# Performance work log

Measured on AMD Instinct MI355X. Metric: run time of the kernel, lower is better.

## Reference

```python
import jax, jax.numpy as jnp
import numpy as np

B, C, H, W = 1, 448, 64, 64
K, M, PAD, STRIDE = 7, 7, 3, 1
CG = C // K          # key/query channels (KeyQueryMap divides by k) = 64
GP_HID = int(0.5 * CG)  # geometry prior hidden channels = 32
K2 = K * K
CENTER = K2 // 2


def conv1x1(x, w, b):
    # x: (B, Cin, H, W), w: (Cout, Cin), b: (Cout,)
    return jnp.einsum('bchw,oc->bohw', x, w) + b[None, :, None, None]


def unfold(x):
    # torch.nn.Unfold(K, dilation=1, padding=PAD, stride=STRIDE)
    # output layout: (B, Cin*K2, L) with dim1 index = c*K2 + (di*K + dj)
    Bc, Cc, Hc, Wc = x.shape
    xp = jnp.pad(x, ((0, 0), (0, 0), (PAD, PAD), (PAD, PAD)))
    Ho = (Hc + 2 * PAD - K) // STRIDE + 1
    Wo = (Wc + 2 * PAD - K) // STRIDE + 1
    patches = [xp[:, :, di:di + Ho * STRIDE:STRIDE, dj:dj + Wo * STRIDE:STRIDE]
               for di in range(K) for dj in range(K)]
    u = jnp.stack(patches, axis=2)  # (B, Cc, K2, Ho, Wo)
    return u.reshape(Bc, Cc * K2, Ho * Wo), Ho, Wo


def geometry_prior(gp_w1, gp_b1, gp_w2, gp_b2):
    ar = jnp.arange(-(K // 2), K // 2 + 1, dtype=jnp.float32)   # -3..3
    x_pos = jnp.broadcast_to(ar[None, :], (K, K))
    y_pos = jnp.broadcast_to(ar[::-1][:, None], (K, K))          # 3..-3 down rows
    pos = jnp.stack([x_pos, y_pos], axis=0)[None]                # (1, 2, K, K)
    h = jax.nn.relu(conv1x1(pos, gp_w1, gp_b1))
    out = conv1x1(h, gp_w2, gp_b2)                               # (1, CG, K, K)
    return out.reshape(1, CG, 1, K2)


def setup_inputs() -> dict:
    key = jax.random.key(0)
    ks = jax.random.split(key, 12)
    def lin(k, cout, cin):
        return jax.random.normal(k, (cout, cin), jnp.float32) / np.sqrt(cin)
    inp = {
        'x': jax.random.normal(ks[0], (B, C, H, W), jnp.float32),
        'Wk': lin(ks[1], CG, C), 'bk': jnp.zeros((CG,), jnp.float32),
        'Wq': lin(ks[2], CG, C), 'bq': jnp.zeros((CG,), jnp.float32),
        'gp_w1': lin(ks[3], GP_HID, 2), 'gp_b1': jax.random.normal(ks[4], (GP_HID,), jnp.float32) * 0.01,
        'gp_w2': lin(ks[5], CG, GP_HID), 'gp_b2': jax.random.normal(ks[6], (CG,), jnp.float32) * 0.01,
        'Wf': lin(ks[7], C, C), 'bf': jnp.zeros((C,), jnp.float32),
    }
    return inp


def reference(x, Wk, bk, Wq, bq, gp_w1, gp_b1, gp_w2, gp_b2, Wf, bf):
    gpk = geometry_prior(gp_w1, gp_b1, gp_w2, gp_b2)        # (1, CG, 1, K2)
    km = conv1x1(x, Wk, bk)                                  # (B, CG, H, W)
    qm = conv1x1(x, Wq, bq)
    ku, Ho, Wo = unfold(km)
    L = Ho * Wo
    ku = ku.reshape(B, CG, L, K2)   # same row-major semantics as torch .view
    qu, _, _ = unfold(qm)
    qu = qu.reshape(B, CG, L, K2)
    ak = ku * qu[:, :, :, CENTER:CENTER + 1]                 # (B, CG, L, K2)
    ck = jax.nn.softmax(ak + gpk, axis=-1)                   # (B, CG, L, K2)
    xu, _, _ = unfold(x)
    xu = xu.reshape(B, M, C // M, L, K2)                     # (B, M, CG, L, K2)
    # ck broadcasts over the M axis (valid since B == 1); sum over window dim
    pre = jnp.einsum('bglp,bmglp->bmgl', ck, xu).reshape(B, C, Ho, Wo)
    return conv1x1(pre, Wf, bf)
```

## Files before the change

### kernel.cpp

```cpp
#include <hip/hip_runtime.h>
#include <hip/hip_bf16.h>

#define CC   448
#define CGC  64
#define MMM  7
#define HWSZ 4096
#define KK2  49
#define GPH  32

typedef __attribute__((ext_vector_type(8))) short   short8;
typedef __attribute__((ext_vector_type(4))) float   f32x4;
typedef __attribute__((ext_vector_type(4))) unsigned short us4;

__device__ __forceinline__ unsigned short f2b(float f) {
    union { __hip_bfloat16 h; unsigned short u; } cv;
    cv.h = __float2bfloat16(f);
    return cv.u;
}

__global__ __launch_bounds__(1024, 4) void kq_mfma(
    const float* __restrict__ x,
    const float* __restrict__ Wk, const float* __restrict__ bk,
    const float* __restrict__ Wq, const float* __restrict__ bq,
    float* __restrict__ km, float* __restrict__ qm)
{
    __shared__ unsigned short As[57344];
    __shared__ unsigned short Bs[7168];
    __shared__ float         red[2048];

    const int tid  = threadIdx.x;
    const int nT   = blockIdx.x * 16;
    const int lane = tid & 63;
    const int wid  = tid >> 6;
    const int l15  = lane & 15;
    const int l4   = lane >> 4;

    #pragma unroll
    for (int i = 0; i < 14; ++i) {
        int idx = tid + i * 1024;
        int row = idx / 112;
        int c   = idx - row * 112;
        const float* src = (row < 64) ? (Wk + (size_t)row * CC)
                                      : (Wq + (size_t)(row - 64) * CC);
        float4 v = *(const float4*)(src + c * 4);
        int kg = c >> 1, jo = (c & 1) * 4;
        *(us4*)&As[kg * 1024 + row * 8 + jo] =
            (us4){ f2b(v.x), f2b(v.y), f2b(v.z), f2b(v.w) };
    }
    #pragma unroll
    for (int i = 0; i < 2; ++i) {
        int idx = tid + i * 1024;
        if (idx < 1792) {
            int row = idx >> 2, c4 = idx & 3;
            float4 v = *(const float4*)(x + (size_t)row * HWSZ + nT + c4 * 4);
            int kg = row >> 3, j = row & 7;
            int b  = kg * 128 + c4 * 32 + j;
            Bs[b]      = f2b(v.x);
            Bs[b + 8]  = f2b(v.y);
            Bs[b + 16] = f2b(v.z);
            Bs[b + 24] = f2b(v.w);
        }
    }
    __syncthreads();

    const int mt = (wid & 7) * 16;
    const int kh = wid >> 3;
    f32x4 acc = (f32x4){0.f, 0.f, 0.f, 0.f};
    #pragma unroll
    for (int i = 0; i < 7; ++i) {
        int K4 = kh * 28 + i * 4;
        short8 fa = *(short8*)&As[(K4 + l4) * 1024 + (mt + l15) * 8];
        short8 fb = *(short8*)&Bs[(K4 + l4) * 128 + l15 * 8];
        acc = __builtin_amdgcn_mfma_f32_16x16x32_bf16(fa, fb, acc, 0, 0, 0);
    }
    if (kh == 1)
        *(f32x4*)&red[(wid & 7) * 256 + lane * 4] = acc;
    __syncthreads();
    if (kh == 0) {
        f32x4 o = *(f32x4*)&red[(wid & 7) * 256 + lane * 4];
        const bool isK = (mt < 64);
        float*       Cd   = isK ? km : qm;
        const float* bias = isK ? bk : bq;
        const int rb = (mt & 63) + l4 * 4;
        #pragma unroll
        for (int r = 0; r < 4; ++r) {
            int row = rb + r;
            Cd[(size_t)row * HWSZ + nT + l15] = acc[r] + o[r] + bias[row];
        }
    }
}

__global__ __launch_bounds__(1024, 4) void fconv_mfma(
    const float* __restrict__ pre,
    const float* __restrict__ Wf, const float* __restrict__ bfv,
    float* __restrict__ out)
{
    __shared__ unsigned short As[50176];
    __shared__ unsigned short Bs[28672];

    const int tid  = threadIdx.x;
    const int bid  = blockIdx.x;
    const int nT   = (bid >> 2) * 64;
    const int oT   = (bid & 3) * 112;
    const int lane = tid & 63;
    const int wid  = tid >> 6;
    const int l15  = lane & 15;
    const int l4   = lane >> 4;

    #pragma unroll
    for (int i = 0; i < 13; ++i) {
        int idx = tid + i * 1024;
        if (idx < 12544) {
            int row = idx / 112;
            int c   = idx - row * 112;
            float4 v = *(const float4*)(Wf + (size_t)(oT + row) * CC + c * 4);
            int kg = c >> 1, jo = (c & 1) * 4;
            *(us4*)&As[kg * 896 + row * 8 + jo] =
                (us4){ f2b(v.x), f2b(v.y), f2b(v.z), f2b(v.w) };
        }
    }
    #pragma unroll
    for (int i = 0; i < 7; ++i) {
        int idx = tid + i * 1024;
        int row = idx >> 4, c4 = idx & 15;
        float4 v = *(const float4*)(pre + (size_t)row * HWSZ + nT + c4 * 4);
        int kg = row >> 3, j = row & 7;
        int b  = kg * 512 + c4 * 32 + j;
        Bs[b]      = f2b(v.x);
        Bs[b + 8]  = f2b(v.y);
        Bs[b + 16] = f2b(v.z);
        Bs[b + 24] = f2b(v.w);
    }
    __syncthreads();

    if (wid < 14) {
        const int mt = (wid % 7) * 16;
        const int np = wid / 7;
        f32x4 a0 = (f32x4){0.f, 0.f, 0.f, 0.f};
        f32x4 a1 = (f32x4){0.f, 0.f, 0.f, 0.f};
        #pragma unroll
        for (int i = 0; i < 14; ++i) {
            int K4 = i * 4;
            short8 fa  = *(short8*)&As[(K4 + l4) * 896 + (mt + l15) * 8];
            short8 fb0 = *(short8*)&Bs[(K4 + l4) * 512 + (np * 32 + l15) * 8];
            short8 fb1 = *(short8*)&Bs[(K4 + l4) * 512 + (np * 32 + 16 + l15) * 8];
            a0 = __builtin_amdgcn_mfma_f32_16x16x32_bf16(fa, fb0, a0, 0, 0, 0);
            a1 = __builtin_amdgcn_mfma_f32_16x16x32_bf16(fa, fb1, a1, 0, 0, 0);
        }
        #pragma unroll
        for (int wn2 = 0; wn2 < 2; ++wn2) {
            const f32x4 a = wn2 ? a1 : a0;
            #pragma unroll
            for (int r = 0; r < 4; ++r) {
                int row = oT + mt + l4 * 4 + r;
                int col = nT + np * 32 + wn2 * 16 + l15;
                out[(size_t)row * HWSZ + col] = a[r] + bfv[row];
            }
        }
    }
}

#define GLO 196
#define GHI 260
#define PGW (GLO + HWSZ + GHI)
#define NPG 8

__global__ __launch_bounds__(1024, 4) void attn_kernel(
    const float* __restrict__ km, const float* __restrict__ qm,
    const float* __restrict__ x,
    const float* __restrict__ gw1, const float* __restrict__ gb1,
    const float* __restrict__ gw2, const float* __restrict__ gb2,
    float* __restrict__ pre)
{
    __shared__ __align__(16) float sm[NPG * PGW];
    __shared__ float gpk_s[KK2];

    const int tid = threadIdx.x;
    const int g   = blockIdx.y;
    const int lp  = blockIdx.x * 1024 + tid;

    if (tid < NPG * 114) {
        int page = tid / 114;
        int r    = tid - page * 114;
        int w    = (r < 49) ? r * 4 : (GLO + HWSZ + (r - 49) * 4);
        *(float4*)&sm[page * PGW + w] = (float4){0.f, 0.f, 0.f, 0.f};
    }
    {
        const float4* s0 = (const float4*)(km + (size_t)g * HWSZ);
        *(float4*)&sm[GLO + tid * 4] = s0[tid];
        #pragma unroll
        for (int m = 0; m < MMM; ++m) {
            const float4* sx = (const float4*)(x + (size_t)(m * CGC + g) * HWSZ);
            *(float4*)&sm[(m + 1) * PGW + GLO + tid * 4] = sx[tid];
        }
    }
    if (tid < KK2) {
        int di = tid / 7, dj = tid - di * 7;
        float xp = (float)(dj - 3);
        float yp = (float)(3 - di);
        float a2 = gb2[g];
        #pragma unroll
        for (int j = 0; j < GPH; ++j) {
            float h = fmaxf(gw1[j * 2 + 0] * xp + gw1[j * 2 + 1] * yp + gb1[j], 0.f);
            a2 = fmaf(gw2[g * GPH + j], h, a2);
        }
        gpk_s[tid] = a2;
    }

    float qc;
    {
        int nc = lp * KK2 + 24;
        int pc = nc >> 12, lc = nc & 4095;
        int dic = (pc * 37) >> 8, djc = pc - dic * 7;
        int i = (lc >> 6) + dic - 3, j = (lc & 63) + djc - 3;
        bool ok = ((unsigned)i < 64u) && ((unsigned)j < 64u);
        qc = ok ? qm[(size_t)g * HWSZ + i * 64 + j] : 0.f;
    }

    const int n0 = lp * KK2;
    const int p0 = n0 >> 12;
    const int l0 = n0 & 4095;
    const int ts = ((p0 + 1) << 12) - n0;
    const int di0 = (p0 * 37) >> 8, dj0 = p0 - di0 * 7;
    const int p1  = p0 + 1;
    const int di1 = (p1 * 37) >> 8, dj1 = p1 - di1 * 7;
    const int dm0 = dj0 - 3, dm1 = dj1 - 3;
    const int B0 = GLO + l0 + (di0 - 3) * 64 + dm0;
    const int B1 = GLO + l0 - HWSZ + (di1 - 3) * 64 + dm1;
    const int c0 = l0 + (dm0 > 0 ? dm0 : 0), w0 = (dm0 < 0) ? -dm0 : dm0;
    const int c1 = l0 + (dm1 > 0 ? dm1 : 0), w1 = (dm1 < 0) ? -dm1 : dm1;

    __syncthreads();

    float d = 0.f;
    float acc[MMM];
    #pragma unroll
    for (int m = 0; m < MMM; ++m) acc[m] = 0.f;

    #pragma unroll
    for (int tp = 0; tp < 24; ++tp) {
        const int t0 = 2 * tp, t1 = t0 + 1;
        const bool s1 = (t1 >= ts);
        const int bb = s1 ? B1 : B0;
        const int cc = s1 ? c1 : c0;
        const int ww = s1 ? w1 : w0;
        float kv0 = sm[bb + t0];
        float kv1 = sm[bb + t1];
        const bool bad0 = (((cc + t0) & 63) < ww);
        const bool bad1 = (((cc + t1) & 63) < ww);
        kv0 = bad0 ? 0.f : kv0;
        kv1 = bad1 ? 0.f : kv1;
        const float e0 = __expf(fmaf(kv0, qc, gpk_s[t0]));
        const float e1 = __expf(fmaf(kv1, qc, gpk_s[t1]));
        d += e0 + e1;
        const float em0 = bad0 ? 0.f : e0;
        const float em1 = bad1 ? 0.f : e1;
        #pragma unroll
        for (int m = 0; m < MMM; ++m) {
            const int ob = bb + (m + 1) * PGW;
            acc[m] = fmaf(em1, sm[ob + t1], fmaf(em0, sm[ob + t0], acc[m]));
        }
    }
    {
        const bool s1 = (48 >= ts);
        const int bb = s1 ? B1 : B0;
        const int cc = s1 ? c1 : c0;
        const int ww = s1 ? w1 : w0;
        float kv = sm[bb + 48];
        const bool bad = (((cc + 48) & 63) < ww);
        kv = bad ? 0.f : kv;
        const float e = __expf(fmaf(kv, qc, gpk_s[48]));
        d += e;
        const float em = bad ? 0.f : e;
        #pragma unroll
        for (int m = 0; m < MMM; ++m)
            acc[m] = fmaf(em, sm[bb + (m + 1) * PGW + 48], acc[m]);
    }
    if (ts < 49 && (ts & 1)) {
        const int tw = ts - 1;
        const float gw = gpk_s[tw];
        float kw = sm[B1 + tw];
        const bool bw = (((c1 + tw) & 63) < w1);
        kw = bw ? 0.f : kw;
        const float ew  = __expf(fmaf(kw, qc, gw));
        const float emw = bw ? 0.f : ew;
        float kr = sm[B0 + tw];
        const bool br = (((c0 + tw) & 63) < w0);
        kr = br ? 0.f : kr;
        const float er  = __expf(fmaf(kr, qc, gw));
        const float emr = br ? 0.f : er;
        d += er - ew;
        #pragma unroll
        for (int m = 0; m < MMM; ++m)
            acc[m] += emr * sm[B0 + (m + 1) * PGW + tw]
                    - emw * sm[B1 + (m + 1) * PGW + tw];
    }

    const float inv = 1.f / d;
    #pragma unroll
    for (int m = 0; m < MMM; ++m)
        pre[(size_t)(m * CGC + g) * HWSZ + lp] = acc[m] * inv;
}

extern "C" void kernel_launch(void* const* d_in, const int* in_sizes, int n_in,
                              void* d_out, int out_size, void* d_ws, size_t ws_size,
                              hipStream_t stream) {
    const float* x   = (const float*)d_in[0];
    const float* Wk  = (const float*)d_in[1];
    const float* bk  = (const float*)d_in[2];
    const float* Wq  = (const float*)d_in[3];
    const float* bq  = (const float*)d_in[4];
    const float* gw1 = (const float*)d_in[5];
    const float* gb1 = (const float*)d_in[6];
    const float* gw2 = (const float*)d_in[7];
    const float* gb2 = (const float*)d_in[8];
    const float* Wf  = (const float*)d_in[9];
    const float* bfv = (const float*)d_in[10];
    float* out = (float*)d_out;

    float* km  = (float*)d_ws;
    float* qm  = km + CGC * HWSZ;
    float* pre = qm + CGC * HWSZ;

    kq_mfma    <<<dim3(256),    1024, 0, stream>>>(x, Wk, bk, Wq, bq, km, qm);
    attn_kernel<<<dim3(4, CGC), 1024, 0, stream>>>(km, qm, x, gw1, gb1, gw2, gb2, pre);
    fconv_mfma <<<dim3(256),    1024, 0, stream>>>(pre, Wf, bfv, out);
}
```

Baseline: 108.0 us.

## Fuse three kernels into one persistent kernel with software grid barriers

Merges the key/query projection, the local attention, and the output projection into a single 256-block kernel, using an atomic ticket barrier between stages. This removes two kernel launch gaps and tail effects. The intermediate attention output is also written as bf16 instead of fp32, which halves that traffic and drops a conversion in the last GEMM. The barrier assumes all 256 blocks of 1024 threads with about 154KB of LDS are co-resident. That is one block per CU on 256 CUs, so it risks deadlock if residency falls short.

```diff
diff --git a/kernel.cpp b/kernel.cpp
--- a/kernel.cpp
+++ b/kernel.cpp
@@ -18,288 +18,303 @@
     return cv.u;
 }
 
-__global__ __launch_bounds__(1024, 4) void kq_mfma(
+__device__ unsigned int g_ticket;
+
+__device__ __forceinline__ void grid_sync() {
+    __syncthreads();
+    if (threadIdx.x == 0) {
+        __threadfence();
+        unsigned arrived = __hip_atomic_fetch_add(&g_ticket, 1u,
+                               __ATOMIC_ACQ_REL, __HIP_MEMORY_SCOPE_AGENT) + 1u;
+        unsigned target = ((arrived + 255u) >> 8) << 8;
+        while (__hip_atomic_load(&g_ticket, __ATOMIC_ACQUIRE,
+                                 __HIP_MEMORY_SCOPE_AGENT) < target)
+            __builtin_amdgcn_s_sleep(2);
+        __threadfence();
+    }
+    __syncthreads();
+}
+
+#define GLO 196
+#define GHI 260
+#define PGW (GLO + HWSZ + GHI)
+#define NPG 8
+
+__global__ __launch_bounds__(1024, 4) void fused_all(
     const float* __restrict__ x,
     const float* __restrict__ Wk, const float* __restrict__ bk,
     const float* __restrict__ Wq, const float* __restrict__ bq,
-    float* __restrict__ km, float* __restrict__ qm)
+    const float* __restrict__ gw1, const float* __restrict__ gb1,
+    const float* __restrict__ gw2, const float* __restrict__ gb2,
+    const float* __restrict__ Wf, const float* __restrict__ bfv,
+    float* __restrict__ km, float* __restrict__ qm,
+    unsigned short* __restrict__ preb,
+    float* __restrict__ out)
 {
-    __shared__ unsigned short As[57344];
-    __shared__ unsigned short Bs[7168];
-    __shared__ float         red[2048];
+    __shared__ __align__(16) unsigned char smem[157696];
 
     const int tid  = threadIdx.x;
-    const int nT   = blockIdx.x * 16;
+    const int bid  = blockIdx.x;
     const int lane = tid & 63;
     const int wid  = tid >> 6;
     const int l15  = lane & 15;
     const int l4   = lane >> 4;
 
-    #pragma unroll
-    for (int i = 0; i < 14; ++i) {
-        int idx = tid + i * 1024;
-        int row = idx / 112;
-        int c   = idx - row * 112;
-        const float* src = (row < 64) ? (Wk + (size_t)row * CC)
-                                      : (Wq + (size_t)(row - 64) * CC);
-        float4 v = *(const float4*)(src + c * 4);
-        int kg = c >> 1, jo = (c & 1) * 4;
-        *(us4*)&As[kg * 1024 + row * 8 + jo] =
-            (us4){ f2b(v.x), f2b(v.y), f2b(v.z), f2b(v.w) };
-    }
-    #pragma unroll
-    for (int i = 0; i < 2; ++i) {
-        int idx = tid + i * 1024;
-        if (idx < 1792) {
-            int row = idx >> 2, c4 = idx & 3;
-            float4 v = *(const float4*)(x + (size_t)row * HWSZ + nT + c4 * 4);
-            int kg = row >> 3, j = row & 7;
-            int b  = kg * 128 + c4 * 32 + j;
-            Bs[b]      = f2b(v.x);
-            Bs[b + 8]  = f2b(v.y);
-            Bs[b + 16] = f2b(v.z);
-            Bs[b + 24] = f2b(v.w);
-        }
-    }
-    __syncthreads();
-
-    const int mt = (wid & 7) * 16;
-    const int kh = wid >> 3;
-    f32x4 acc = (f32x4){0.f, 0.f, 0.f, 0.f};
-    #pragma unroll
-    for (int i = 0; i < 7; ++i) {
-        int K4 = kh * 28 + i * 4;
-        short8 fa = *(short8*)&As[(K4 + l4) * 1024 + (mt + l15) * 8];
-        short8 fb = *(short8*)&Bs[(K4 + l4) * 128 + l15 * 8];
-        acc = __builtin_amdgcn_mfma_f32_16x16x32_bf16(fa, fb, acc, 0, 0, 0);
-    }
-    if (kh == 1)
-        *(f32x4*)&red[(wid & 7) * 256 + lane * 4] = acc;
-    __syncthreads();
-    if (kh == 0) {
-        f32x4 o = *(f32x4*)&red[(wid & 7) * 256 + lane * 4];
-        const bool isK = (mt < 64);
-        float*       Cd   = isK ? km : qm;
-        const float* bias = isK ? bk : bq;
-        const int rb = (mt & 63) + l4 * 4;
-        #pragma unroll
-        for (int r = 0; r < 4; ++r) {
-            int row = rb + r;
-            Cd[(size_t)row * HWSZ + nT + l15] = acc[r] + o[r] + bias[row];
-        }
-    }
-}
-
-__global__ __launch_bounds__(1024, 4) void fconv_mfma(
-    const float* __restrict__ pre,
-    const float* __restrict__ Wf, const float* __restrict__ bfv,
-    float* __restrict__ out)
-{
-    __shared__ unsigned short As[50176];
-    __shared__ unsigned short Bs[28672];
-
-    const int tid  = threadIdx.x;
-    const int bid  = blockIdx.x;
-    const int nT   = (bid >> 2) * 64;
-    const int oT   = (bid & 3) * 112;
-    const int lane = tid & 63;
-    const int wid  = tid >> 6;
-    const int l15  = lane & 15;
-    const int l4   = lane >> 4;
-
-    #pragma unroll
-    for (int i = 0; i < 13; ++i) {
-        int idx = tid + i * 1024;
-        if (idx < 12544) {
+    {
+        unsigned short* As  = (unsigned short*)smem;
+        unsigned short* Bs  = As + 57344;
+        float*          red = (float*)(Bs + 7168);
+
+        const int nT = bid * 16;
+
+        #pragma unroll
+        for (int i = 0; i < 14; ++i) {
+            int idx = tid + i * 1024;
             int row = idx / 112;
             int c   = idx - row * 112;
-            float4 v = *(const float4*)(Wf + (size_t)(oT + row) * CC + c * 4);
+            const float* src = (row < 64) ? (Wk + (size_t)row * CC)
+                                          : (Wq + (size_t)(row - 64) * CC);
+            float4 v = *(const float4*)(src + c * 4);
             int kg = c >> 1, jo = (c & 1) * 4;
-            *(us4*)&As[kg * 896 + row * 8 + jo] =
+            *(us4*)&As[kg * 1024 + row * 8 + jo] =
                 (us4){ f2b(v.x), f2b(v.y), f2b(v.z), f2b(v.w) };
         }
+        #pragma unroll
+        for (int i = 0; i < 2; ++i) {
+            int idx = tid + i * 1024;
+            if (idx < 1792) {
+                int row = idx >> 2, c4 = idx & 3;
+                float4 v = *(const float4*)(x + (size_t)row * HWSZ + nT + c4 * 4);
+                int kg = row >> 3, j = row & 7;
+                int b  = kg * 128 + c4 * 32 + j;
+                Bs[b]      = f2b(v.x);
+                Bs[b + 8]  = f2b(v.y);
+                Bs[b + 16] = f2b(v.z);
+                Bs[b + 24] = f2b(v.w);
+            }
+        }
+        __syncthreads();
+
+        const int mt = (wid & 7) * 16;
+        const int kh = wid >> 3;
+        f32x4 acc = (f32x4){0.f, 0.f, 0.f, 0.f};
+        #pragma unroll
+        for (int i = 0; i < 7; ++i) {
+            int K4 = kh * 28 + i * 4;
+            short8 fa = *(short8*)&As[(K4 + l4) * 1024 + (mt + l15) * 8];
+            short8 fb = *(short8*)&Bs[(K4 + l4) * 128 + l15 * 8];
+            acc = __builtin_amdgcn_mfma_f32_16x16x32_bf16(fa, fb, acc, 0, 0, 0);
+        }
+        if (kh == 1)
+            *(f32x4*)&red[(wid & 7) * 256 + lane * 4] = acc;
+        __syncthreads();
+        if (kh == 0) {
+            f32x4 o = *(f32x4*)&red[(wid & 7) * 256 + lane * 4];
+            const bool isK = (mt < 64);
+            float*       Cd   = isK ? km : qm;
+            const float* bias = isK ? bk : bq;
+            const int rb = (mt & 63) + l4 * 4;
+            #pragma unroll
+            for (int r = 0; r < 4; ++r) {
+                int row = rb + r;
+                Cd[(size_t)row * HWSZ + nT + l15] = acc[r] + o[r] + bias[row];
+            }
+        }
     }
-    #pragma unroll
-    for (int i = 0; i < 7; ++i) {
-        int idx = tid + i * 1024;
-        int row = idx >> 4, c4 = idx & 15;
-        float4 v = *(const float4*)(pre + (size_t)row * HWSZ + nT + c4 * 4);
-        int kg = row >> 3, j = row & 7;
-        int b  = kg * 512 + c4 * 32 + j;
-        Bs[b]      = f2b(v.x);
-        Bs[b + 8]  = f2b(v.y);
-        Bs[b + 16] = f2b(v.z);
-        Bs[b + 24] = f2b(v.w);
+
+    grid_sync();
+
+    {
+        float* sm    = (float*)smem;
+        float* gpk_s = sm + NPG * PGW;
+
+        const int g  = bid & 63;
+        const int lp = (bid >> 6) * 1024 + tid;
+
+        if (tid < NPG * 114) {
+            int page = tid / 114;
+            int r    = tid - page * 114;
+            int w    = (r < 49) ? r * 4 : (GLO + HWSZ + (r - 49) * 4);
+            *(float4*)&sm[page * PGW + w] = (float4){0.f, 0.f, 0.f, 0.f};
+        }
+        {
+            const float4* s0 = (const float4*)(km + (size_t)g * HWSZ);
+            *(float4*)&sm[GLO + tid * 4] = s0[tid];
+            #pragma unroll
+            for (int m = 0; m < MMM; ++m) {
+                const float4* sx = (const float4*)(x + (size_t)(m * CGC + g) * HWSZ);
+                *(float4*)&sm[(m + 1) * PGW + GLO + tid * 4] = sx[tid];
+            }
+        }
+        if (tid < KK2) {
+            int di = tid / 7, dj = tid - di * 7;
+            float xp = (float)(dj - 3);
+            float yp = (float)(3 - di);
+            float a2 = gb2[g];
+            #pragma unroll
+            for (int j = 0; j < GPH; ++j) {
+                float h = fmaxf(gw1[j * 2 + 0] * xp + gw1[j * 2 + 1] * yp + gb1[j], 0.f);
+                a2 = fmaf(gw2[g * GPH + j], h, a2);
+            }
+            gpk_s[tid] = a2;
+        }
+
+        float qc;
+        {
+            int nc = lp * KK2 + 24;
+            int pc = nc >> 12, lc = nc & 4095;
+            int dic = (pc * 37) >> 8, djc = pc - dic * 7;
+            int i = (lc >> 6) + dic - 3, j = (lc & 63) + djc - 3;
+            bool ok = ((unsigned)i < 64u) && ((unsigned)j < 64u);
+            qc = ok ? qm[(size_t)g * HWSZ + i * 64 + j] : 0.f;
+        }
+
+        const int n0 = lp * KK2;
+        const int p0 = n0 >> 12;
+        const int l0 = n0 & 4095;
+        const int ts = ((p0 + 1) << 12) - n0;
+        const int di0 = (p0 * 37) >> 8, dj0 = p0 - di0 * 7;
+        const int p1  = p0 + 1;
+        const int di1 = (p1 * 37) >> 8, dj1 = p1 - di1 * 7;
+        const int dm0 = dj0 - 3, dm1 = dj1 - 3;
+        const int B0 = GLO + l0 + (di0 - 3) * 64 + dm0;
+        const int B1 = GLO + l0 - HWSZ + (di1 - 3) * 64 + dm1;
+        const int c0 = l0 + (dm0 > 0 ? dm0 : 0), w0 = (dm0 < 0) ? -dm0 : dm0;
+        const int c1 = l0 + (dm1 > 0 ? dm1 : 0), w1 = (dm1 < 0) ? -dm1 : dm1;
+
+        __syncthreads();
+
+        float d = 0.f;
+        float acc[MMM];
+        #pragma unroll
+        for (int m = 0; m < MMM; ++m) acc[m] = 0.f;
+
+        #pragma unroll
+        for (int tp = 0; tp < 24; ++tp) {
+            const int t0 = 2 * tp, t1 = t0 + 1;
+            const bool s1 = (t1 >= ts);
+            const int bb = s1 ? B1 : B0;
+            const int cc = s1 ? c1 : c0;
+            const int ww = s1 ? w1 : w0;
+            float kv0 = sm[bb + t0];
+            float kv1 = sm[bb + t1];
+            const bool bad0 = (((cc + t0) & 63) < ww);
+            const bool bad1 = (((cc + t1) & 63) < ww);
+            kv0 = bad0 ? 0.f : kv0;
+            kv1 = bad1 ? 0.f : kv1;
+            const float e0 = __expf(fmaf(kv0, qc, gpk_s[t0]));
+            const float e1 = __expf(fmaf(kv1, qc, gpk_s[t1]));
+            d += e0 + e1;
+            const float em0 = bad0 ? 0.f : e0;
+            const float em1 = bad1 ? 0.f : e1;
+            #pragma unroll
+            for (int m = 0; m < MMM; ++m) {
+                const int ob = bb + (m + 1) * PGW;
+                acc[m] = fmaf(em1, sm[ob + t1], fmaf(em0, sm[ob + t0], acc[m]));
+            }
+        }
+        {
+            const bool s1 = (48 >= ts);
+            const int bb = s1 ? B1 : B0;
+            const int cc = s1 ? c1 : c0;
+            const int ww = s1 ? w1 : w0;
+            float kv = sm[bb + 48];
+            const bool bad = (((cc + 48) & 63) < ww);
+            kv = bad ? 0.f : kv;
+            const float e = __expf(fmaf(kv, qc, gpk_s[48]));
+            d += e;
+            const float em = bad ? 0.f : e;
+            #pragma unroll
+            for (int m = 0; m < MMM; ++m)
+                acc[m] = fmaf(em, sm[bb + (m + 1) * PGW + 48], acc[m]);
+        }
+        if (ts < 49 && (ts & 1)) {
+            const int tw = ts - 1;
+            const float gw = gpk_s[tw];
+            float kw = sm[B1 + tw];
+            const bool bw = (((c1 + tw) & 63) < w1);
+            kw = bw ? 0.f : kw;
+            const float ew  = __expf(fmaf(kw, qc, gw));
+            const float emw = bw ? 0.f : ew;
+            float kr = sm[B0 + tw];
+            const bool br = (((c0 + tw) & 63) < w0);
+            kr = br ? 0.f : kr;
+            const float er  = __expf(fmaf(kr, qc, gw));
+            const float emr = br ? 0.f : er;
+            d += er - ew;
+            #pragma unroll
+            for (int m = 0; m < MMM; ++m)
+                acc[m] += emr * sm[B0 + (m + 1) * PGW + tw]
+                        - emw * sm[B1 + (m + 1) * PGW + tw];
+        }
+
+        const float inv = 1.f / d;
+        #pragma unroll
+        for (int m = 0; m < MMM; ++m)
+            preb[(size_t)(m * CGC + g) * HWSZ + lp] = f2b(acc[m] * inv);
     }
-    __syncthreads();
-
-    if (wid < 14) {
-        const int mt = (wid % 7) * 16;
-        const int np = wid / 7;
-        f32x4 a0 = (f32x4){0.f, 0.f, 0.f, 0.f};
-        f32x4 a1 = (f32x4){0.f, 0.f, 0.f, 0.f};
-        #pragma unroll
-        for (int i = 0; i < 14; ++i) {
-            int K4 = i * 4;
-            short8 fa  = *(short8*)&As[(K4 + l4) * 896 + (mt + l15) * 8];
-            short8 fb0 = *(short8*)&Bs[(K4 + l4) * 512 + (np * 32 + l15) * 8];
-            short8 fb1 = *(short8*)&Bs[(K4 + l4) * 512 + (np * 32 + 16 + l15) * 8];
-            a0 = __builtin_amdgcn_mfma_f32_16x16x32_bf16(fa, fb0, a0, 0, 0, 0);
-            a1 = __builtin_amdgcn_mfma_f32_16x16x32_bf16(fa, fb1, a1, 0, 0, 0);
-        }
-        #pragma unroll
-        for (int wn2 = 0; wn2 < 2; ++wn2) {
-            const f32x4 a = wn2 ? a1 : a0;
-            #pragma unroll
-            for (int r = 0; r < 4; ++r) {
-                int row = oT + mt + l4 * 4 + r;
-                int col = nT + np * 32 + wn2 * 16 + l15;
-                out[(size_t)row * HWSZ + col] = a[r] + bfv[row];
+
+    grid_sync();
+
+    {
+        unsigned short* As = (unsigned short*)smem;
+        unsigned short* Bs = As + 50176;
+
+        const int nT = (bid >> 2) * 64;
+        const int oT = (bid & 3) * 112;
+
+        #pragma unroll
+        for (int i = 0; i < 13; ++i) {
+            int idx = tid + i * 1024;
+            if (idx < 12544) {
+                int row = idx / 112;
+                int c   = idx - row * 112;
+                float4 v = *(const float4*)(Wf + (size_t)(oT + row) * CC + c * 4);
+                int kg = c >> 1, jo = (c & 1) * 4;
+                *(us4*)&As[kg * 896 + row * 8 + jo] =
+                    (us4){ f2b(v.x), f2b(v.y), f2b(v.z), f2b(v.w) };
+            }
+        }
+        #pragma unroll
+        for (int i = 0; i < 7; ++i) {
+            int idx = tid + i * 1024;
+            int row = idx >> 4, c4 = idx & 15;
+            us4 v = *(const us4*)(preb + (size_t)row * HWSZ + nT + c4 * 4);
+            int kg = row >> 3, j = row & 7;
+            int b  = kg * 512 + c4 * 32 + j;
+            Bs[b]      = v.x;
+            Bs[b + 8]  = v.y;
+            Bs[b + 16] = v.z;
+            Bs[b + 24] = v.w;
+        }
+        __syncthreads();
+
+        if (wid < 14) {
+            const int mt = (wid % 7) * 16;
+            const int np = wid / 7;
+            f32x4 a0 = (f32x4){0.f, 0.f, 0.f, 0.f};
+            f32x4 a1 = (f32x4){0.f, 0.f, 0.f, 0.f};
+            #pragma unroll
+            for (int i = 0; i < 14; ++i) {
+                int K4 = i * 4;
+                short8 fa  = *(short8*)&As[(K4 + l4) * 896 + (mt + l15) * 8];
+                short8 fb0 = *(short8*)&Bs[(K4 + l4) * 512 + (np * 32 + l15) * 8];
+                short8 fb1 = *(short8*)&Bs[(K4 + l4) * 512 + (np * 32 + 16 + l15) * 8];
+                a0 = __builtin_amdgcn_mfma_f32_16x16x32_bf16(fa, fb0, a0, 0, 0, 0);
+                a1 = __builtin_amdgcn_mfma_f32_16x16x32_bf16(fa, fb1, a1, 0, 0, 0);
+            }
+            #pragma unroll
+            for (int wn2 = 0; wn2 < 2; ++wn2) {
+                const f32x4 a = wn2 ? a1 : a0;
+                #pragma unroll
+                for (int r = 0; r < 4; ++r) {
+                    int row = oT + mt + l4 * 4 + r;
+                    int col = nT + np * 32 + wn2 * 16 + l15;
+                    out[(size_t)row * HWSZ + col] = a[r] + bfv[row];
+                }
             }
         }
     }
-}
-
-#define GLO 196
-#define GHI 260
-#define PGW (GLO + HWSZ + GHI)
-#define NPG 8
-
-__global__ __launch_bounds__(1024, 4) void attn_kernel(
-    const float* __restrict__ km, const float* __restrict__ qm,
-    const float* __restrict__ x,
-    const float* __restrict__ gw1, const float* __restrict__ gb1,
-    const float* __restrict__ gw2, const float* __restrict__ gb2,
-    float* __restrict__ pre)
-{
-    __shared__ __align__(16) float sm[NPG * PGW];
-    __shared__ float gpk_s[KK2];
-
-    const int tid = threadIdx.x;
-    const int g   = blockIdx.y;
-    const int lp  = blockIdx.x * 1024 + tid;
-
-    if (tid < NPG * 114) {
-        int page = tid / 114;
-        int r    = tid - page * 114;
-        int w    = (r < 49) ? r * 4 : (GLO + HWSZ + (r - 49) * 4);
-        *(float4*)&sm[page * PGW + w] = (float4){0.f, 0.f, 0.f, 0.f};
-    }
-    {
-        const float4* s0 = (const float4*)(km + (size_t)g * HWSZ);
-        *(float4*)&sm[GLO + tid * 4] = s0[tid];
-        #pragma unroll
-        for (int m = 0; m < MMM; ++m) {
-            const float4* sx = (const float4*)(x + (size_t)(m * CGC + g) * HWSZ);
-            *(float4*)&sm[(m + 1) * PGW + GLO + tid * 4] = sx[tid];
-        }
-    }
-    if (tid < KK2) {
-        int di = tid / 7, dj = tid - di * 7;
-        float xp = (float)(dj - 3);
-        float yp = (float)(3 - di);
-        float a2 = gb2[g];
-        #pragma unroll
-        for (int j = 0; j < GPH; ++j) {
-            float h = fmaxf(gw1[j * 2 + 0] * xp + gw1[j * 2 + 1] * yp + gb1[j], 0.f);
-            a2 = fmaf(gw2[g * GPH + j], h, a2);
-        }
-        gpk_s[tid] = a2;
-    }
-
-    float qc;
-    {
-        int nc = lp * KK2 + 24;
-        int pc = nc >> 12, lc = nc & 4095;
-        int dic = (pc * 37) >> 8, djc = pc - dic * 7;
-        int i = (lc >> 6) + dic - 3, j = (lc & 63) + djc - 3;
-        bool ok = ((unsigned)i < 64u) && ((unsigned)j < 64u);
-        qc = ok ? qm[(size_t)g * HWSZ + i * 64 + j] : 0.f;
-    }
-
-    const int n0 = lp * KK2;
-    const int p0 = n0 >> 12;
-    const int l0 = n0 & 4095;
-    const int ts = ((p0 + 1) << 12) - n0;
-    const int di0 = (p0 * 37) >> 8, dj0 = p0 - di0 * 7;
-    const int p1  = p0 + 1;
-    const int di1 = (p1 * 37) >> 8, dj1 = p1 - di1 * 7;
-    const int dm0 = dj0 - 3, dm1 = dj1 - 3;
-    const int B0 = GLO + l0 + (di0 - 3) * 64 + dm0;
-    const int B1 = GLO + l0 - HWSZ + (di1 - 3) * 64 + dm1;
-    const int c0 = l0 + (dm0 > 0 ? dm0 : 0), w0 = (dm0 < 0) ? -dm0 : dm0;
-    const int c1 = l0 + (dm1 > 0 ? dm1 : 0), w1 = (dm1 < 0) ? -dm1 : dm1;
-
-    __syncthreads();
-
-    float d = 0.f;
-    float acc[MMM];
-    #pragma unroll
-    for (int m = 0; m < MMM; ++m) acc[m] = 0.f;
-
-    #pragma unroll
-    for (int tp = 0; tp < 24; ++tp) {
-        const int t0 = 2 * tp, t1 = t0 + 1;
-        const bool s1 = (t1 >= ts);
-        const int bb = s1 ? B1 : B0;
-        const int cc = s1 ? c1 : c0;
-        const int ww = s1 ? w1 : w0;
-        float kv0 = sm[bb + t0];
-        float kv1 = sm[bb + t1];
-        const bool bad0 = (((cc + t0) & 63) < ww);
-        const bool bad1 = (((cc + t1) & 63) < ww);
-        kv0 = bad0 ? 0.f : kv0;
-        kv1 = bad1 ? 0.f : kv1;
-        const float e0 = __expf(fmaf(kv0, qc, gpk_s[t0]));
-        const float e1 = __expf(fmaf(kv1, qc, gpk_s[t1]));
-        d += e0 + e1;
-        const float em0 = bad0 ? 0.f : e0;
-        const float em1 = bad1 ? 0.f : e1;
-        #pragma unroll
-        for (int m = 0; m < MMM; ++m) {
-            const int ob = bb + (m + 1) * PGW;
-            acc[m] = fmaf(em1, sm[ob + t1], fmaf(em0, sm[ob + t0], acc[m]));
-        }
-    }
-    {
-        const bool s1 = (48 >= ts);
-        const int bb = s1 ? B1 : B0;
-        const int cc = s1 ? c1 : c0;
-        const int ww = s1 ? w1 : w0;
-        float kv = sm[bb + 48];
-        const bool bad = (((cc + 48) & 63) < ww);
-        kv = bad ? 0.f : kv;
-        const float e = __expf(fmaf(kv, qc, gpk_s[48]));
-        d += e;
-        const float em = bad ? 0.f : e;
-        #pragma unroll
-        for (int m = 0; m < MMM; ++m)
-            acc[m] = fmaf(em, sm[bb + (m + 1) * PGW + 48], acc[m]);
-    }
-    if (ts < 49 && (ts & 1)) {
-        const int tw = ts - 1;
-        const float gw = gpk_s[tw];
-        float kw = sm[B1 + tw];
-        const bool bw = (((c1 + tw) & 63) < w1);
-        kw = bw ? 0.f : kw;
-        const float ew  = __expf(fmaf(kw, qc, gw));
-        const float emw = bw ? 0.f : ew;
-        float kr = sm[B0 + tw];
-        const bool br = (((c0 + tw) & 63) < w0);
-        kr = br ? 0.f : kr;
-        const float er  = __expf(fmaf(kr, qc, gw));
-        const float emr = br ? 0.f : er;
-        d += er - ew;
-        #pragma unroll
-        for (int m = 0; m < MMM; ++m)
-            acc[m] += emr * sm[B0 + (m + 1) * PGW + tw]
-                    - emw * sm[B1 + (m + 1) * PGW + tw];
-    }
-
-    const float inv = 1.f / d;
-    #pragma unroll
-    for (int m = 0; m < MMM; ++m)
-        pre[(size_t)(m * CGC + g) * HWSZ + lp] = acc[m] * inv;
 }
 
 extern "C" void kernel_launch(void* const* d_in, const int* in_sizes, int n_in,
@@ -320,9 +335,8 @@
 
     float* km  = (float*)d_ws;
     float* qm  = km + CGC * HWSZ;
-    float* pre = qm + CGC * HWSZ;
-
-    kq_mfma    <<<dim3(256),    1024, 0, stream>>>(x, Wk, bk, Wq, bq, km, qm);
-    attn_kernel<<<dim3(4, CGC), 1024, 0, stream>>>(km, qm, x, gw1, gb1, gw2, gb2, pre);
-    fconv_mfma <<<dim3(256),    1024, 0, stream>>>(pre, Wf, bfv, out);
+    unsigned short* preb = (unsigned short*)(qm + CGC * HWSZ);
+
+    fused_all<<<dim3(256), 1024, 0, stream>>>(
+        x, Wk, bk, Wq, bq, gw1, gb1, gw2, gb2, Wf, bfv, km, qm, preb, out);
 }
```

New measurement: 160.6 us. +48.7%, slower.
